# Kernel tuning notes

Hardware: AMD Instinct MI355X
Metric: run time of the kernel (lower is better)

The kernel has to match this reference:

```python
import jax, jax.numpy as jnp
import numpy as np

NUM_FREQS = 10
EPS = 1e-6


def _posenc(x):
    # NeRF positional encoding with identity: [x, sin(2^i x), cos(2^i x)]
    freqs = 2.0 ** jnp.arange(NUM_FREQS, dtype=x.dtype)  # [L]
    xb = x[..., None, :] * freqs[:, None]                # [..., L, D]
    four = jnp.sin(jnp.concatenate([xb, xb + 0.5 * jnp.pi], axis=-2))
    return jnp.concatenate([x, four.reshape(*x.shape[:-1], -1)], axis=-1)


def _ln(x, s, b):
    mu = jnp.mean(x, axis=-1, keepdims=True)
    var = jnp.mean(jnp.square(x - mu), axis=-1, keepdims=True)
    return (x - mu) * jax.lax.rsqrt(var + EPS) * s + b


def _layer(net, chunk, hW, hb, hls, hlb, wW, wb, bW, bb_, ls, lb):
    # hyper net (hyper_depth=1): Dense -> LayerNorm -> relu
    h = jax.nn.relu(_ln(chunk @ hW + hb, hls, hlb))
    n_in = net.shape[-1]
    n_out = bb_.shape[-1]
    # generate per-point weight matrix [K,P,N,M] and bias [K,P,N]
    w = (h @ wW + wb).reshape(*h.shape[:-1], n_out, n_in)
    b = h @ bW + bb_
    net = jnp.einsum('kpm,kpnm->kpn', net, w) + b
    return jax.nn.relu(_ln(net, ls, lb))


def _forward(rays, latent_tokens, token_embeddings, h_W0, h_b0, h_ln_s0, h_ln_b0,
             w_W0, w_b0, bb_W0, bb_b0, ln_s0, ln_b0,
             h_W, h_b, h_ln_s, h_ln_b, w_W, w_b, bb_W, bb_b, ln_s, ln_b,
             rgb_W, rgb_b):
    origins = rays[..., 0:3]
    dirs = rays[..., 3:6]
    plucker = jnp.concatenate([dirs, jnp.cross(origins, dirs)], axis=-1)  # [K,P,6]
    net = _posenc(plucker)  # [K,P,126]

    K, T, Z = latent_tokens.shape
    emb = jnp.broadcast_to(token_embeddings[None], (K, T, token_embeddings.shape[-1]))
    lt = jnp.concatenate([latent_tokens, emb], axis=-1).reshape(K, 1, -1)  # [K,1,T*(Z+E)]
    P = rays.shape[1]
    latent = jnp.broadcast_to(lt, (K, P, lt.shape[-1]))
    skips = jnp.split(latent, 8, axis=-1)  # 8 chunks of [K,P,128]

    net = _layer(net, skips[0], h_W0, h_b0, h_ln_s0, h_ln_b0,
                 w_W0, w_b0, bb_W0, bb_b0, ln_s0, ln_b0)
    for i in range(7):
        net = _layer(net, skips[i + 1], h_W[i], h_b[i], h_ln_s[i], h_ln_b[i],
                     w_W[i], w_b[i], bb_W[i], bb_b[i], ln_s[i], ln_b[i])
    return jax.nn.sigmoid(net @ rgb_W + rgb_b)


def setup_inputs() -> dict:
    key = jax.random.key(0)
    ks = jax.random.split(key, 12)
    K, P, T, Z, W = 2, 4096, 8, 64, 64
    IN0 = 6 * (1 + 2 * NUM_FREQS)  # 126
    f32 = jnp.float32
    d = {}
    d['rays'] = jax.random.normal(ks[0], (K, P, 6), f32)
    d['latent_tokens'] = jax.random.normal(ks[1], (K, T, Z), f32)
    d['token_embeddings'] = jax.random.normal(ks[2], (T, 64), f32)
    # layer 0 (input dim 126)
    d['h_W0'] = jax.random.normal(ks[3], (Z + 64, W), f32)
    d['h_b0'] = jnp.zeros((W,), f32)
    d['h_ln_s0'] = jnp.ones((W,), f32)
    d['h_ln_b0'] = jnp.zeros((W,), f32)
    d['w_W0'] = jax.random.normal(ks[4], (W, IN0 * W), f32)
    d['w_b0'] = jnp.zeros((IN0 * W,), f32)
    d['bb_W0'] = jax.random.normal(ks[5], (W, W), f32)
    d['bb_b0'] = jnp.zeros((W,), f32)
    d['ln_s0'] = jnp.ones((W,), f32)
    d['ln_b0'] = jnp.zeros((W,), f32)
    # layers 1..7 (input dim 64), stacked
    L = 7
    d['h_W'] = jax.random.normal(ks[6], (L, Z + 64, W), f32)
    d['h_b'] = jnp.zeros((L, W), f32)
    d['h_ln_s'] = jnp.ones((L, W), f32)
    d['h_ln_b'] = jnp.zeros((L, W), f32)
    d['w_W'] = jax.random.normal(ks[7], (L, W, W * W), f32)
    d['w_b'] = jnp.zeros((L, W * W), f32)
    d['bb_W'] = jax.random.normal(ks[8], (L, W, W), f32)
    d['bb_b'] = jnp.zeros((L, W), f32)
    d['ln_s'] = jnp.ones((L, W), f32)
    d['ln_b'] = jnp.zeros((L, W), f32)
    d['rgb_W'] = jax.random.normal(ks[9], (W, 3), f32)
    d['rgb_b'] = jnp.zeros((3,), f32)
    return d


def reference(rays, latent_tokens, token_embeddings, h_W0, h_b0, h_ln_s0, h_ln_b0,
              w_W0, w_b0, bb_W0, bb_b0, ln_s0, ln_b0,
              h_W, h_b, h_ln_s, h_ln_b, w_W, w_b, bb_W, bb_b, ln_s, ln_b,
              rgb_W, rgb_b):
    return _forward(rays, latent_tokens, token_embeddings, h_W0, h_b0, h_ln_s0, h_ln_b0,
                    w_W0, w_b0, bb_W0, bb_b0, ln_s0, ln_b0,
                    h_W, h_b, h_ln_s, h_ln_b, w_W, w_b, bb_W, bb_b, ln_s, ln_b,
                    rgb_W, rgb_b)
```

## Files before the change

### kernel.cpp

```cpp
#include <hip/hip_runtime.h>
#include <math.h>

#define EPSF 1e-6f
#define RPW 4

__device__ __forceinline__ float rl(float v, int srclane) {
    return __uint_as_float(__builtin_amdgcn_readlane(__float_as_uint(v), srclane));
}

__device__ __forceinline__ float wave_sum64(float v) {
#pragma unroll
    for (int off = 32; off > 0; off >>= 1) v += __shfl_xor(v, off, 64);
    return v;
}

__device__ __forceinline__ float ln_relu(float a, float s, float b) {
    float mu  = wave_sum64(a) * (1.0f / 64.0f);
    float d   = a - mu;
    float var = wave_sum64(d * d) * (1.0f / 64.0f);
    return fmaxf(d * rsqrtf(var + EPSF) * s + b, 0.0f);
}

__device__ __forceinline__ float posenc_elem(const float* pl, int e) {
    if (e < 6) return pl[e];
    int t = e - 6;
    int j = t / 6;
    int i = t - j * 6;
    int jm = (j < 10) ? j : (j - 10);
    float arg = pl[i] * (float)(1 << jm);
    if (j >= 10) arg += 1.5707963705062866f;
    return sinf(arg);
}

__global__ __launch_bounds__(256) void precompute_kernel(
    const float* __restrict__ latent_tokens, const float* __restrict__ token_embeddings,
    const float* __restrict__ h_W0, const float* __restrict__ h_b0,
    const float* __restrict__ h_ln_s0, const float* __restrict__ h_ln_b0,
    const float* __restrict__ w_W0, const float* __restrict__ w_b0,
    const float* __restrict__ bb_W0, const float* __restrict__ bb_b0,
    const float* __restrict__ h_W, const float* __restrict__ h_b,
    const float* __restrict__ h_ln_s, const float* __restrict__ h_ln_b,
    const float* __restrict__ w_W, const float* __restrict__ w_b,
    const float* __restrict__ bb_W, const float* __restrict__ bb_b,
    float* __restrict__ ws, int offW, int offB)
{
    const int s = blockIdx.x;
    const int l = blockIdx.y;
    const int k = blockIdx.z;
    const int tid = threadIdx.x;

    __shared__ float s_chunk[128];
    __shared__ float s_h[64];

    if (tid < 128) {
        s_chunk[tid] = (tid < 64) ? latent_tokens[(k * 8 + l) * 64 + tid]
                                  : token_embeddings[l * 64 + (tid - 64)];
    }
    __syncthreads();

    const float* hW  = (l == 0) ? h_W0    : h_W    + (size_t)(l - 1) * 128 * 64;
    const float* hb  = (l == 0) ? h_b0    : h_b    + (l - 1) * 64;
    const float* hls = (l == 0) ? h_ln_s0 : h_ln_s + (l - 1) * 64;
    const float* hlb = (l == 0) ? h_ln_b0 : h_ln_b + (l - 1) * 64;

    if (tid < 64) {
        float acc = hb[tid];
#pragma unroll 16
        for (int m = 0; m < 128; m++) acc += s_chunk[m] * hW[m * 64 + tid];
        float mu  = wave_sum64(acc) * (1.0f / 64.0f);
        float d   = acc - mu;
        float var = wave_sum64(d * d) * (1.0f / 64.0f);
        float y   = d * rsqrtf(var + EPSF) * hls[tid] + hlb[tid];
        s_h[tid]  = fmaxf(y, 0.0f);
    }
    __syncthreads();

    const int n_in  = (l == 0) ? 126 : 64;
    const int nflat = 64 * n_in;
    const int slice = nflat / 16;
    const int o0 = s * slice;
    const float* wW = (l == 0) ? w_W0 : w_W + (size_t)(l - 1) * 64 * 4096;
    const float* wb = (l == 0) ? w_b0 : w_b + (size_t)(l - 1) * 4096;
    float* Wt = (l == 0) ? ws + (size_t)k * 8192
                         : ws + offW + ((size_t)k * 7 + (l - 1)) * 4096;

    for (int o = o0 + tid; o < o0 + slice; o += 256) {
        float acc = wb[o];
#pragma unroll 8
        for (int j = 0; j < 64; j++) acc += s_h[j] * wW[j * nflat + o];
        if (l == 0) {
            int n = o / 126;
            int m = o - n * 126;
            Wt[n * 128 + m] = acc;
        } else {
            Wt[o] = acc;
        }
    }

    if (l == 0 && s == 0 && tid < 128) {
        Wt[(tid >> 1) * 128 + 126 + (tid & 1)] = 0.0f;
    }

    if (s == 0 && tid < 64) {
        const float* bW  = (l == 0) ? bb_W0 : bb_W + (size_t)(l - 1) * 64 * 64;
        const float* bb_ = (l == 0) ? bb_b0 : bb_b + (l - 1) * 64;
        float acc = bb_[tid];
#pragma unroll 8
        for (int j = 0; j < 64; j++) acc += s_h[j] * bW[j * 64 + tid];
        ws[offB + (k * 8 + l) * 64 + tid] = acc;
    }
}

__global__ __launch_bounds__(256) void forward_kernel(
    const float* __restrict__ rays,
    const float* __restrict__ ln_s0, const float* __restrict__ ln_b0,
    const float* __restrict__ ln_s, const float* __restrict__ ln_b,
    const float* __restrict__ rgb_W, const float* __restrict__ rgb_b,
    const float* __restrict__ ws, int offW, int offB,
    float* __restrict__ out, int K, int P)
{
    const int warp = threadIdx.x >> 6;
    const int lane = threadIdx.x & 63;
    const int total = K * P;
    const int r0 = (blockIdx.x * 4 + warp) * RPW;
    if (r0 >= total) return;
    const int k = r0 / P;

    float net0[RPW], net1[RPW];
#pragma unroll
    for (int q = 0; q < RPW; q++) {
        int r = r0 + q; if (r > total - 1) r = total - 1;
        float o0 = rays[r * 6 + 0], o1 = rays[r * 6 + 1], o2 = rays[r * 6 + 2];
        float d0 = rays[r * 6 + 3], d1 = rays[r * 6 + 4], d2 = rays[r * 6 + 5];
        float pl[6];
        pl[0] = d0; pl[1] = d1; pl[2] = d2;
        pl[3] = o1 * d2 - o2 * d1;
        pl[4] = o2 * d0 - o0 * d2;
        pl[5] = o0 * d1 - o1 * d0;
        net0[q] = posenc_elem(pl, lane);
        net1[q] = (lane + 64 < 126) ? posenc_elem(pl, lane + 64) : 0.0f;
    }

    float acc[RPW];

    {
        const float4* row = (const float4*)(ws + (size_t)k * 8192 + lane * 128);
        float bia = ws[offB + (k * 8 + 0) * 64 + lane];
#pragma unroll
        for (int q = 0; q < RPW; q++) acc[q] = bia;

        float4 w4[16];
#pragma unroll
        for (int j = 0; j < 16; j++) w4[j] = row[j];
#pragma unroll
        for (int m = 0; m < 64; m++) {
            float wm = ((const float*)w4)[m];
#pragma unroll
            for (int q = 0; q < RPW; q++) acc[q] += rl(net0[q], m) * wm;
        }
#pragma unroll
        for (int j = 0; j < 16; j++) w4[j] = row[16 + j];
#pragma unroll
        for (int m = 0; m < 64; m++) {
            float wm = ((const float*)w4)[m];
#pragma unroll
            for (int q = 0; q < RPW; q++) acc[q] += rl(net1[q], m) * wm;
        }
        float s = ln_s0[lane], b = ln_b0[lane];
#pragma unroll
        for (int q = 0; q < RPW; q++) acc[q] = ln_relu(acc[q], s, b);
    }

#pragma unroll 1
    for (int l = 1; l < 8; l++) {
        const float4* row = (const float4*)(ws + offW + ((size_t)k * 7 + (l - 1)) * 4096 + lane * 64);
        float bia = ws[offB + (k * 8 + l) * 64 + lane];
        float4 w4[16];
#pragma unroll
        for (int j = 0; j < 16; j++) w4[j] = row[j];
        float na[RPW];
#pragma unroll
        for (int q = 0; q < RPW; q++) na[q] = bia;
#pragma unroll
        for (int m = 0; m < 64; m++) {
            float wm = ((const float*)w4)[m];
#pragma unroll
            for (int q = 0; q < RPW; q++) na[q] += rl(acc[q], m) * wm;
        }
        float s = ln_s[(l - 1) * 64 + lane], b = ln_b[(l - 1) * 64 + lane];
#pragma unroll
        for (int q = 0; q < RPW; q++) acc[q] = ln_relu(na[q], s, b);
    }

    float w0 = rgb_W[lane * 3 + 0], w1 = rgb_W[lane * 3 + 1], w2 = rgb_W[lane * 3 + 2];
    float b0 = rgb_b[0], b1 = rgb_b[1], b2 = rgb_b[2];
#pragma unroll
    for (int q = 0; q < RPW; q++) {
        float c0 = wave_sum64(acc[q] * w0);
        float c1 = wave_sum64(acc[q] * w1);
        float c2 = wave_sum64(acc[q] * w2);
        if (lane == 0 && r0 + q < total) {
            out[(r0 + q) * 3 + 0] = 1.0f / (1.0f + expf(-(c0 + b0)));
            out[(r0 + q) * 3 + 1] = 1.0f / (1.0f + expf(-(c1 + b1)));
            out[(r0 + q) * 3 + 2] = 1.0f / (1.0f + expf(-(c2 + b2)));
        }
    }
}

extern "C" void kernel_launch(void* const* d_in, const int* in_sizes, int n_in,
                              void* d_out, int out_size, void* d_ws, size_t ws_size,
                              hipStream_t stream) {
    const float* rays    = (const float*)d_in[0];
    const float* latent  = (const float*)d_in[1];
    const float* tok_emb = (const float*)d_in[2];
    const float* h_W0    = (const float*)d_in[3];
    const float* h_b0    = (const float*)d_in[4];
    const float* h_ln_s0 = (const float*)d_in[5];
    const float* h_ln_b0 = (const float*)d_in[6];
    const float* w_W0    = (const float*)d_in[7];
    const float* w_b0    = (const float*)d_in[8];
    const float* bb_W0   = (const float*)d_in[9];
    const float* bb_b0   = (const float*)d_in[10];
    const float* ln_s0   = (const float*)d_in[11];
    const float* ln_b0   = (const float*)d_in[12];
    const float* h_W     = (const float*)d_in[13];
    const float* h_b     = (const float*)d_in[14];
    const float* h_ln_s  = (const float*)d_in[15];
    const float* h_ln_b  = (const float*)d_in[16];
    const float* w_W     = (const float*)d_in[17];
    const float* w_b     = (const float*)d_in[18];
    const float* bb_W    = (const float*)d_in[19];
    const float* bb_b    = (const float*)d_in[20];
    const float* ln_s    = (const float*)d_in[21];
    const float* ln_b    = (const float*)d_in[22];
    const float* rgb_W   = (const float*)d_in[23];
    const float* rgb_b   = (const float*)d_in[24];
    float* out = (float*)d_out;

    const int K = in_sizes[1] / (8 * 64);
    const int P = in_sizes[0] / (6 * K);
    const int offW = K * 8192;
    const int offB = offW + K * 7 * 4096;

    float* ws = (float*)d_ws;

    dim3 pgrid(16, 8, K);
    precompute_kernel<<<pgrid, 256, 0, stream>>>(
        latent, tok_emb, h_W0, h_b0, h_ln_s0, h_ln_b0, w_W0, w_b0, bb_W0, bb_b0,
        h_W, h_b, h_ln_s, h_ln_b, w_W, w_b, bb_W, bb_b, ws, offW, offB);

    const int total = K * P;
    const int rays_per_block = 4 * RPW;
    const int blocks = (total + rays_per_block - 1) / rays_per_block;
    forward_kernel<<<blocks, 256, 0, stream>>>(
        rays, ln_s0, ln_b0, ln_s, ln_b, rgb_W, rgb_b,
        ws, offW, offB, out, K, P);
}
```

Baseline: 159.4 us.

## Prefetch next layer weights, single-pass LayerNorm stats, finer precompute grid

The forward kernel now loads the next layer's per-point weight row into registers while the current layer's LayerNorm runs, and loads both halves of layer 0's weights up front, to hide global-load latency. LayerNorm mean and variance now come from one fused shuffle reduction of sum and sum of squares, which halves the reduction passes but is less numerically robust. The precompute kernel is split into twice as many smaller 128-thread blocks with deeper unrolling to raise parallelism. Launch bounds now request 3 waves-per-block occupancy, and the extra prefetch buffers raise register pressure.

```diff
diff --git a/kernel.cpp b/kernel.cpp
--- a/kernel.cpp
+++ b/kernel.cpp
@@ -14,11 +14,16 @@
     return v;
 }
 
-__device__ __forceinline__ float ln_relu(float a, float s, float b) {
-    float mu  = wave_sum64(a) * (1.0f / 64.0f);
-    float d   = a - mu;
-    float var = wave_sum64(d * d) * (1.0f / 64.0f);
-    return fmaxf(d * rsqrtf(var + EPSF) * s + b, 0.0f);
+__device__ __forceinline__ void ln_stats(float a, float& mu, float& rstd) {
+    float s1 = a, s2 = a * a;
+#pragma unroll
+    for (int off = 32; off > 0; off >>= 1) {
+        s1 += __shfl_xor(s1, off, 64);
+        s2 += __shfl_xor(s2, off, 64);
+    }
+    mu = s1 * (1.0f / 64.0f);
+    float var = fmaxf(s2 * (1.0f / 64.0f) - mu * mu, 0.0f);
+    rstd = rsqrtf(var + EPSF);
 }
 
 __device__ __forceinline__ float posenc_elem(const float* pl, int e) {
@@ -32,7 +37,7 @@
     return sinf(arg);
 }
 
-__global__ __launch_bounds__(256) void precompute_kernel(
+__global__ __launch_bounds__(128, 4) void precompute_kernel(
     const float* __restrict__ latent_tokens, const float* __restrict__ token_embeddings,
     const float* __restrict__ h_W0, const float* __restrict__ h_b0,
     const float* __restrict__ h_ln_s0, const float* __restrict__ h_ln_b0,
@@ -52,10 +57,8 @@
     __shared__ float s_chunk[128];
     __shared__ float s_h[64];
 
-    if (tid < 128) {
-        s_chunk[tid] = (tid < 64) ? latent_tokens[(k * 8 + l) * 64 + tid]
-                                  : token_embeddings[l * 64 + (tid - 64)];
-    }
+    s_chunk[tid] = (tid < 64) ? latent_tokens[(k * 8 + l) * 64 + tid]
+                              : token_embeddings[l * 64 + (tid - 64)];
     __syncthreads();
 
     const float* hW  = (l == 0) ? h_W0    : h_W    + (size_t)(l - 1) * 128 * 64;
@@ -67,26 +70,25 @@
         float acc = hb[tid];
 #pragma unroll 16
         for (int m = 0; m < 128; m++) acc += s_chunk[m] * hW[m * 64 + tid];
-        float mu  = wave_sum64(acc) * (1.0f / 64.0f);
-        float d   = acc - mu;
-        float var = wave_sum64(d * d) * (1.0f / 64.0f);
-        float y   = d * rsqrtf(var + EPSF) * hls[tid] + hlb[tid];
-        s_h[tid]  = fmaxf(y, 0.0f);
+        float mu, rstd;
+        ln_stats(acc, mu, rstd);
+        float y = (acc - mu) * rstd * hls[tid] + hlb[tid];
+        s_h[tid] = fmaxf(y, 0.0f);
     }
     __syncthreads();
 
     const int n_in  = (l == 0) ? 126 : 64;
     const int nflat = 64 * n_in;
-    const int slice = nflat / 16;
+    const int slice = nflat / 32;
     const int o0 = s * slice;
     const float* wW = (l == 0) ? w_W0 : w_W + (size_t)(l - 1) * 64 * 4096;
     const float* wb = (l == 0) ? w_b0 : w_b + (size_t)(l - 1) * 4096;
     float* Wt = (l == 0) ? ws + (size_t)k * 8192
                          : ws + offW + ((size_t)k * 7 + (l - 1)) * 4096;
 
-    for (int o = o0 + tid; o < o0 + slice; o += 256) {
+    for (int o = o0 + tid; o < o0 + slice; o += 128) {
         float acc = wb[o];
-#pragma unroll 8
+#pragma unroll 16
         for (int j = 0; j < 64; j++) acc += s_h[j] * wW[j * nflat + o];
         if (l == 0) {
             int n = o / 126;
@@ -97,7 +99,7 @@
         }
     }
 
-    if (l == 0 && s == 0 && tid < 128) {
+    if (l == 0 && s == 0) {
         Wt[(tid >> 1) * 128 + 126 + (tid & 1)] = 0.0f;
     }
 
@@ -105,13 +107,13 @@
         const float* bW  = (l == 0) ? bb_W0 : bb_W + (size_t)(l - 1) * 64 * 64;
         const float* bb_ = (l == 0) ? bb_b0 : bb_b + (l - 1) * 64;
         float acc = bb_[tid];
-#pragma unroll 8
+#pragma unroll 16
         for (int j = 0; j < 64; j++) acc += s_h[j] * bW[j * 64 + tid];
         ws[offB + (k * 8 + l) * 64 + tid] = acc;
     }
 }
 
-__global__ __launch_bounds__(256) void forward_kernel(
+__global__ __launch_bounds__(256, 3) void forward_kernel(
     const float* __restrict__ rays,
     const float* __restrict__ ln_s0, const float* __restrict__ ln_b0,
     const float* __restrict__ ln_s, const float* __restrict__ ln_b,
@@ -141,55 +143,70 @@
         net1[q] = (lane + 64 < 126) ? posenc_elem(pl, lane + 64) : 0.0f;
     }
 
+    const float* WL = ws + offW + (size_t)k * 7 * 4096;
     float acc[RPW];
+    float4 w4[16];
 
     {
         const float4* row = (const float4*)(ws + (size_t)k * 8192 + lane * 128);
+        float4 w4b[16];
+#pragma unroll
+        for (int j = 0; j < 16; j++) w4[j]  = row[j];
+#pragma unroll
+        for (int j = 0; j < 16; j++) w4b[j] = row[16 + j];
         float bia = ws[offB + (k * 8 + 0) * 64 + lane];
-#pragma unroll
-        for (int q = 0; q < RPW; q++) acc[q] = bia;
-
-        float4 w4[16];
-#pragma unroll
-        for (int j = 0; j < 16; j++) w4[j] = row[j];
+        float pre[RPW];
+#pragma unroll
+        for (int q = 0; q < RPW; q++) pre[q] = bia;
 #pragma unroll
         for (int m = 0; m < 64; m++) {
             float wm = ((const float*)w4)[m];
 #pragma unroll
-            for (int q = 0; q < RPW; q++) acc[q] += rl(net0[q], m) * wm;
-        }
-#pragma unroll
-        for (int j = 0; j < 16; j++) w4[j] = row[16 + j];
+            for (int q = 0; q < RPW; q++) pre[q] += rl(net0[q], m) * wm;
+        }
+#pragma unroll
+        for (int m = 0; m < 64; m++) {
+            float wm = ((const float*)w4b)[m];
+#pragma unroll
+            for (int q = 0; q < RPW; q++) pre[q] += rl(net1[q], m) * wm;
+        }
+        const float4* nrow = (const float4*)(WL + lane * 64);
+#pragma unroll
+        for (int j = 0; j < 16; j++) w4[j] = nrow[j];
+        float s = ln_s0[lane], b = ln_b0[lane];
+#pragma unroll
+        for (int q = 0; q < RPW; q++) {
+            float mu, rstd;
+            ln_stats(pre[q], mu, rstd);
+            acc[q] = fmaxf((pre[q] - mu) * rstd * s + b, 0.0f);
+        }
+    }
+
+#pragma unroll 1
+    for (int l = 1; l < 8; l++) {
+        float na[RPW];
+        float bia = ws[offB + (k * 8 + l) * 64 + lane];
+#pragma unroll
+        for (int q = 0; q < RPW; q++) na[q] = bia;
 #pragma unroll
         for (int m = 0; m < 64; m++) {
             float wm = ((const float*)w4)[m];
 #pragma unroll
-            for (int q = 0; q < RPW; q++) acc[q] += rl(net1[q], m) * wm;
-        }
-        float s = ln_s0[lane], b = ln_b0[lane];
-#pragma unroll
-        for (int q = 0; q < RPW; q++) acc[q] = ln_relu(acc[q], s, b);
-    }
-
-#pragma unroll 1
-    for (int l = 1; l < 8; l++) {
-        const float4* row = (const float4*)(ws + offW + ((size_t)k * 7 + (l - 1)) * 4096 + lane * 64);
-        float bia = ws[offB + (k * 8 + l) * 64 + lane];
-        float4 w4[16];
-#pragma unroll
-        for (int j = 0; j < 16; j++) w4[j] = row[j];
-        float na[RPW];
-#pragma unroll
-        for (int q = 0; q < RPW; q++) na[q] = bia;
-#pragma unroll
-        for (int m = 0; m < 64; m++) {
-            float wm = ((const float*)w4)[m];
-#pragma unroll
             for (int q = 0; q < RPW; q++) na[q] += rl(acc[q], m) * wm;
         }
+        {
+            int lp = (l < 7) ? l : 6;
+            const float4* nrow = (const float4*)(WL + (size_t)lp * 4096 + lane * 64);
+#pragma unroll
+            for (int j = 0; j < 16; j++) w4[j] = nrow[j];
+        }
         float s = ln_s[(l - 1) * 64 + lane], b = ln_b[(l - 1) * 64 + lane];
 #pragma unroll
-        for (int q = 0; q < RPW; q++) acc[q] = ln_relu(na[q], s, b);
+        for (int q = 0; q < RPW; q++) {
+            float mu, rstd;
+            ln_stats(na[q], mu, rstd);
+            acc[q] = fmaxf((na[q] - mu) * rstd * s + b, 0.0f);
+        }
     }
 
     float w0 = rgb_W[lane * 3 + 0], w1 = rgb_W[lane * 3 + 1], w2 = rgb_W[lane * 3 + 2];
@@ -244,8 +261,8 @@
 
     float* ws = (float*)d_ws;
 
-    dim3 pgrid(16, 8, K);
-    precompute_kernel<<<pgrid, 256, 0, stream>>>(
+    dim3 pgrid(32, 8, K);
+    precompute_kernel<<<pgrid, 128, 0, stream>>>(
         latent, tok_emb, h_W0, h_b0, h_ln_s0, h_ln_b0, w_W0, w_b0, bb_W0, bb_b0,
         h_W, h_b, h_ln_s, h_ln_b, w_W, w_b, bb_W, bb_b, ws, offW, offB);
 
```

Measured after the change: 157.0 us. Within noise of the previous version (-1.5%).
